# Performance work log

Hardware: AMD Instinct MI355X
Metric: run time of the kernel (lower is better)

Reference implementation:

```python
import jax, jax.numpy as jnp
import numpy as np

N_NODES = 50000   # batch_size * n_verts
N_EDGES = 800000
D_FEAT = 128
UNITS = 256


def setup_inputs() -> dict:
    key = jax.random.key(0)
    k1, k2, k3, k4, k5 = jax.random.split(key, 5)
    features = jax.random.normal(k1, (N_NODES, D_FEAT), dtype=jnp.float32)
    edge_row = jax.random.randint(k2, (N_EDGES,), 0, N_NODES, dtype=jnp.int32)
    edge_col = jax.random.randint(k3, (N_EDGES,), 0, N_NODES, dtype=jnp.int32)
    edge_val = jax.random.uniform(k4, (N_EDGES,), dtype=jnp.float32)
    W = jax.random.normal(k5, (D_FEAT, UNITS), dtype=jnp.float32) * (1.0 / np.sqrt(D_FEAT))
    return {"features": features, "edge_row": edge_row, "edge_col": edge_col,
            "edge_val": edge_val, "W": W}


def reference(features, edge_row, edge_col, edge_val, W):
    # features: [N, F] (already the (batch*n_verts, F) layout the layer reshapes to)
    # A in COO: A[edge_row[e], edge_col[e]] = edge_val[e]
    n = features.shape[0]
    # in_degree = row-sum of A values, +1 for self loop
    in_degree = jax.ops.segment_sum(edge_val, edge_row, num_segments=n) + 1.0
    invsqrt_deg = jax.lax.rsqrt(in_degree)                       # [N]
    normalized = invsqrt_deg[:, None] * features                 # [N, F]
    # pooled = A @ normalized  (gather source rows, scale, scatter-add to dest)
    msgs = edge_val[:, None] * normalized[edge_col]              # [E, F]
    pooled = jax.ops.segment_sum(msgs, edge_row, num_segments=n) # [N, F]
    # self-loop contribution (normalized case)
    pooled = pooled + invsqrt_deg[:, None] * normalized
    # dense projection + relu
    out = jax.nn.relu(pooled @ W)                                # [N, units]
    return out
```

## Files before the change

### kernel.cpp

```cpp
#include <hip/hip_runtime.h>

constexpr int N = 50000;
constexpr int E = 800000;
constexpr int F = 128;
constexpr int U = 256;

constexpr int R      = 8;
constexpr int CAP    = 16;
constexpr int ROWCAP = R * CAP;
constexpr int EBLK2  = (E + 511) / 512;

typedef __attribute__((ext_vector_type(8))) short short8;
typedef __attribute__((ext_vector_type(4))) float float4v;

__device__ inline unsigned short f32_to_bf16(float x) {
    unsigned int u = __float_as_uint(x);
    unsigned int r = (u + 0x7fffu + ((u >> 16) & 1u)) >> 16;
    return (unsigned short)r;
}
__device__ inline float bf_lo(unsigned int u) { return __uint_as_float(u << 16); }
__device__ inline float bf_hi(unsigned int u) { return __uint_as_float(u & 0xffff0000u); }

__global__ __launch_bounds__(256) void hist_kernel(const int* __restrict__ erow,
                                                   const int* __restrict__ ecol,
                                                   const float* __restrict__ eval,
                                                   int* __restrict__ cnt,
                                                   int2* __restrict__ csr,
                                                   const float* __restrict__ W,
                                                   unsigned short* __restrict__ Wt) {
    if (blockIdx.x >= EBLK2) {
        int idx = (blockIdx.x - EBLK2) * 256 + threadIdx.x;
        int k = idx >> 8;
        int n = idx & 255;
        Wt[n * F + k] = f32_to_bf16(W[idx]);
        return;
    }
    int e0  = blockIdx.x * 512 + threadIdx.x;
    int e1  = e0 + 256;
    int rep = blockIdx.x & (R - 1);
    bool h1 = (e1 < E);

    int   r0 = erow[e0];
    int   r1 = h1 ? erow[e1] : 0;
    int   c0 = ecol[e0];
    int   c1 = h1 ? ecol[e1] : 0;
    float v0 = eval[e0];
    float v1 = h1 ? eval[e1] : 0.f;

    int rk0 = atomicAdd(&cnt[r0 * R + rep], 1);
    int rk1 = h1 ? atomicAdd(&cnt[r1 * R + rep], 1) : CAP;

    if (rk0 < CAP)
        csr[(size_t)r0 * ROWCAP + rep * CAP + rk0] = make_int2(c0, __float_as_int(v0));
    if (rk1 < CAP)
        csr[(size_t)r1 * ROWCAP + rep * CAP + rk1] = make_int2(c1, __float_as_int(v1));
}

__global__ __launch_bounds__(256) void norm_kernel(const float* __restrict__ feat,
                                                   const int* __restrict__ cnt,
                                                   int2* __restrict__ csr,
                                                   int2* __restrict__ meta,
                                                   unsigned int* __restrict__ nrm) {
    int gtid = blockIdx.x * 256 + threadIdx.x;
    int n    = gtid >> 6;
    int lane = threadIdx.x & 63;
    if (n >= N) return;

    int s = lane >> 3;
    int j = lane & 7;

    int cval = min(cnt[n * R + (lane & 7)], CAP);
    int tot = 0, myoff = 0, cs = 0;
    #pragma unroll
    for (int t = 0; t < 8; ++t) {
        int ct = __shfl(cval, t, 64);
        tot += ct;
        if (t < s) myoff += ct;
        if (t == s) cs = ct;
    }

    int2* base = csr + (size_t)n * ROWCAP;
    bool h0 = j < cs;
    bool h1 = (j + 8) < cs;
    int2 v0 = h0 ? base[s * CAP + j] : make_int2(0, 0);
    int2 v1 = h1 ? base[s * CAP + 8 + j] : make_int2(0, 0);

    float sum = (h0 ? __int_as_float(v0.y) : 0.f) + (h1 ? __int_as_float(v1.y) : 0.f);
    #pragma unroll
    for (int off = 32; off > 0; off >>= 1) sum += __shfl_xor(sum, off, 64);
    float iv_ = rsqrtf(sum + 1.0f);

    if (h0) base[myoff + j] = v0;
    if (h1) base[myoff + 8 + j] = v1;

    if (lane == 0) meta[n] = make_int2(tot, __float_as_int(iv_));

    float2 f = ((const float2*)feat)[n * 64 + lane];
    nrm[n * 64 + lane] =
        (unsigned int)f32_to_bf16(iv_ * f.x) | ((unsigned int)f32_to_bf16(iv_ * f.y) << 16);
}

__global__ __launch_bounds__(256) void gather_kernel(const int2* __restrict__ meta,
                                                     const int2* __restrict__ csr,
                                                     const unsigned int* __restrict__ nrm,
                                                     unsigned int* __restrict__ pooledb) {
    int gtid = blockIdx.x * 256 + threadIdx.x;
    int n    = gtid >> 6;
    int lane = threadIdx.x & 63;
    if (n >= N) return;

    int2 m = meta[n];
    int tot = m.x;
    float iv_ = __int_as_float(m.y);

    unsigned int self = nrm[n * 64 + lane];
    float acc0 = iv_ * bf_lo(self);
    float acc1 = iv_ * bf_hi(self);

    const int2* base = csr + (size_t)n * ROWCAP;

    int e = 0;
    for (; e + 7 < tot; e += 8) {
        int2 p0 = base[e + 0], p1 = base[e + 1], p2 = base[e + 2], p3 = base[e + 3];
        int2 p4 = base[e + 4], p5 = base[e + 5], p6 = base[e + 6], p7 = base[e + 7];
        unsigned int u0 = nrm[(size_t)p0.x * 64 + lane];
        unsigned int u1 = nrm[(size_t)p1.x * 64 + lane];
        unsigned int u2 = nrm[(size_t)p2.x * 64 + lane];
        unsigned int u3 = nrm[(size_t)p3.x * 64 + lane];
        unsigned int u4 = nrm[(size_t)p4.x * 64 + lane];
        unsigned int u5 = nrm[(size_t)p5.x * 64 + lane];
        unsigned int u6 = nrm[(size_t)p6.x * 64 + lane];
        unsigned int u7 = nrm[(size_t)p7.x * 64 + lane];
        acc0 += __int_as_float(p0.y) * bf_lo(u0); acc1 += __int_as_float(p0.y) * bf_hi(u0);
        acc0 += __int_as_float(p1.y) * bf_lo(u1); acc1 += __int_as_float(p1.y) * bf_hi(u1);
        acc0 += __int_as_float(p2.y) * bf_lo(u2); acc1 += __int_as_float(p2.y) * bf_hi(u2);
        acc0 += __int_as_float(p3.y) * bf_lo(u3); acc1 += __int_as_float(p3.y) * bf_hi(u3);
        acc0 += __int_as_float(p4.y) * bf_lo(u4); acc1 += __int_as_float(p4.y) * bf_hi(u4);
        acc0 += __int_as_float(p5.y) * bf_lo(u5); acc1 += __int_as_float(p5.y) * bf_hi(u5);
        acc0 += __int_as_float(p6.y) * bf_lo(u6); acc1 += __int_as_float(p6.y) * bf_hi(u6);
        acc0 += __int_as_float(p7.y) * bf_lo(u7); acc1 += __int_as_float(p7.y) * bf_hi(u7);
    }
    for (; e + 3 < tot; e += 4) {
        int2 p0 = base[e + 0], p1 = base[e + 1], p2 = base[e + 2], p3 = base[e + 3];
        unsigned int u0 = nrm[(size_t)p0.x * 64 + lane];
        unsigned int u1 = nrm[(size_t)p1.x * 64 + lane];
        unsigned int u2 = nrm[(size_t)p2.x * 64 + lane];
        unsigned int u3 = nrm[(size_t)p3.x * 64 + lane];
        acc0 += __int_as_float(p0.y) * bf_lo(u0); acc1 += __int_as_float(p0.y) * bf_hi(u0);
        acc0 += __int_as_float(p1.y) * bf_lo(u1); acc1 += __int_as_float(p1.y) * bf_hi(u1);
        acc0 += __int_as_float(p2.y) * bf_lo(u2); acc1 += __int_as_float(p2.y) * bf_hi(u2);
        acc0 += __int_as_float(p3.y) * bf_lo(u3); acc1 += __int_as_float(p3.y) * bf_hi(u3);
    }
    for (; e < tot; ++e) {
        int2 p0 = base[e];
        unsigned int u0 = nrm[(size_t)p0.x * 64 + lane];
        acc0 += __int_as_float(p0.y) * bf_lo(u0);
        acc1 += __int_as_float(p0.y) * bf_hi(u0);
    }
    pooledb[n * 64 + lane] =
        (unsigned int)f32_to_bf16(acc0) | ((unsigned int)f32_to_bf16(acc1) << 16);
}

__global__ __launch_bounds__(256) void gemm_mfma_kernel(const unsigned short* __restrict__ Ab,
                                                        const unsigned short* __restrict__ Wt,
                                                        float* __restrict__ out) {
    __shared__ unsigned short As[16384];
    __shared__ unsigned short Bs[16384];
    const int tid = threadIdx.x;
    const int m0 = blockIdx.x * 128;
    const int n0 = blockIdx.y * 128;

    {
        const int r = tid >> 1;
        const int h = tid & 1;
        const int grow = m0 + r;
        const uint4* asrc = (grow < N) ? (const uint4*)(Ab + (size_t)grow * F) : nullptr;
        const uint4* bsrc = (const uint4*)(Wt + (size_t)(n0 + r) * F);
        #pragma unroll
        for (int j = 0; j < 8; ++j) {
            int o = h * 8 + j;
            int ks = o >> 2, quad = o & 3;
            int slot = ((ks * 8 + (r >> 4)) * 64) + (quad << 4) + (r & 15);
            uint4 av = asrc ? asrc[o] : make_uint4(0u, 0u, 0u, 0u);
            ((uint4*)As)[slot] = av;
            ((uint4*)Bs)[slot] = bsrc[o];
        }
    }
    __syncthreads();

    const int wave = tid >> 6;
    const int lane = tid & 63;
    float4v acc[8][2];
    #pragma unroll
    for (int i = 0; i < 8; ++i) {
        acc[i][0] = (float4v){0.f, 0.f, 0.f, 0.f};
        acc[i][1] = (float4v){0.f, 0.f, 0.f, 0.f};
    }

    #pragma unroll
    for (int ks = 0; ks < 4; ++ks) {
        short8 b0 = *(const short8*)&Bs[(((ks * 8 + wave * 2 + 0) * 64) + lane) * 8];
        short8 b1 = *(const short8*)&Bs[(((ks * 8 + wave * 2 + 1) * 64) + lane) * 8];
        #pragma unroll
        for (int mt = 0; mt < 8; ++mt) {
            short8 a = *(const short8*)&As[(((ks * 8 + mt) * 64) + lane) * 8];
            acc[mt][0] = __builtin_amdgcn_mfma_f32_16x16x32_bf16(a, b0, acc[mt][0], 0, 0, 0);
            acc[mt][1] = __builtin_amdgcn_mfma_f32_16x16x32_bf16(a, b1, acc[mt][1], 0, 0, 0);
        }
    }

    const int quad = lane >> 4;
    const int colt = lane & 15;
    #pragma unroll
    for (int mt = 0; mt < 8; ++mt) {
        #pragma unroll
        for (int nt = 0; nt < 2; ++nt) {
            int col = n0 + (wave * 2 + nt) * 16 + colt;
            #pragma unroll
            for (int i = 0; i < 4; ++i) {
                int row = m0 + mt * 16 + quad * 4 + i;
                if (row < N) out[(size_t)row * U + col] = fmaxf(acc[mt][nt][i], 0.f);
            }
        }
    }
}

extern "C" void kernel_launch(void* const* d_in, const int* in_sizes, int n_in,
                              void* d_out, int out_size, void* d_ws, size_t ws_size,
                              hipStream_t stream) {
    (void)in_sizes; (void)n_in; (void)out_size; (void)ws_size;

    const float* feat = (const float*)d_in[0];
    const int*   erow = (const int*)d_in[1];
    const int*   ecol = (const int*)d_in[2];
    const float* eval = (const float*)d_in[3];
    const float* W    = (const float*)d_in[4];
    float* out = (float*)d_out;

    char* ws = (char*)d_ws;
    int*            cnt     = (int*)  (ws + 0);
    int2*           meta    = (int2*) (ws + 1600000);
    unsigned short* Wt      = (unsigned short*)(ws + 2000000);
    unsigned int*   nrm     = (unsigned int*)  (ws + 2065536);
    unsigned int*   pooledb = (unsigned int*)  (ws + 14865536);
    int2*           csr     = (int2*) (ws + 27665536);

    (void)hipMemsetAsync(cnt, 0, (size_t)N * R * sizeof(int), stream);

    hist_kernel<<<EBLK2 + (F * U) / 256, 256, 0, stream>>>(erow, ecol, eval, cnt, csr, W, Wt);
    norm_kernel  <<<(N * 64) / 256, 256, 0, stream>>>(feat, cnt, csr, meta, nrm);
    gather_kernel<<<(N * 64) / 256, 256, 0, stream>>>(meta, csr, nrm, pooledb);

    dim3 ggrid((N + 127) / 128, U / 128);
    gemm_mfma_kernel<<<ggrid, 256, 0, stream>>>((const unsigned short*)pooledb, Wt, out);
}
```

Measured before the change: 211.9 us.

## Gather with 16-byte vector loads over four edge groups and wave shuffle reduction

The gather kernel now splits each 64-lane wavefront into four groups of 16 lanes. Each group handles a different edge and loads a full 256-byte feature row as uint4 per lane, then the partial sums are combined with xor shuffles. This cuts the number of memory instructions per edge and keeps more independent gathers in flight, at the cost of eight accumulators per lane and a shuffle reduction. The hist kernel also goes back to one edge per thread, which changes the replica assignment and launches twice as many blocks.

```diff
diff --git a/kernel.cpp b/kernel.cpp
--- a/kernel.cpp
+++ b/kernel.cpp
@@ -8,7 +8,7 @@
 constexpr int R      = 8;
 constexpr int CAP    = 16;
 constexpr int ROWCAP = R * CAP;
-constexpr int EBLK2  = (E + 511) / 512;
+constexpr int EBLK   = E / 256;
 
 typedef __attribute__((ext_vector_type(8))) short short8;
 typedef __attribute__((ext_vector_type(4))) float float4v;
@@ -28,32 +28,21 @@
                                                    int2* __restrict__ csr,
                                                    const float* __restrict__ W,
                                                    unsigned short* __restrict__ Wt) {
-    if (blockIdx.x >= EBLK2) {
-        int idx = (blockIdx.x - EBLK2) * 256 + threadIdx.x;
+    if (blockIdx.x >= EBLK) {
+        int idx = (blockIdx.x - EBLK) * 256 + threadIdx.x;
         int k = idx >> 8;
         int n = idx & 255;
         Wt[n * F + k] = f32_to_bf16(W[idx]);
         return;
     }
-    int e0  = blockIdx.x * 512 + threadIdx.x;
-    int e1  = e0 + 256;
+    int e   = blockIdx.x * 256 + threadIdx.x;
+    int row = erow[e];
+    int col = ecol[e];
+    float v = eval[e];
     int rep = blockIdx.x & (R - 1);
-    bool h1 = (e1 < E);
-
-    int   r0 = erow[e0];
-    int   r1 = h1 ? erow[e1] : 0;
-    int   c0 = ecol[e0];
-    int   c1 = h1 ? ecol[e1] : 0;
-    float v0 = eval[e0];
-    float v1 = h1 ? eval[e1] : 0.f;
-
-    int rk0 = atomicAdd(&cnt[r0 * R + rep], 1);
-    int rk1 = h1 ? atomicAdd(&cnt[r1 * R + rep], 1) : CAP;
-
-    if (rk0 < CAP)
-        csr[(size_t)r0 * ROWCAP + rep * CAP + rk0] = make_int2(c0, __float_as_int(v0));
-    if (rk1 < CAP)
-        csr[(size_t)r1 * ROWCAP + rep * CAP + rk1] = make_int2(c1, __float_as_int(v1));
+    int rk  = atomicAdd(&cnt[row * R + rep], 1);
+    if (rk < CAP)
+        csr[(size_t)row * ROWCAP + rep * CAP + rk] = make_int2(col, __float_as_int(v));
 }
 
 __global__ __launch_bounds__(256) void norm_kernel(const float* __restrict__ feat,
@@ -109,56 +98,68 @@
     int lane = threadIdx.x & 63;
     if (n >= N) return;
 
+    int q = lane >> 4;
+    int f = lane & 15;
+
     int2 m = meta[n];
     int tot = m.x;
     float iv_ = __int_as_float(m.y);
 
-    unsigned int self = nrm[n * 64 + lane];
-    float acc0 = iv_ * bf_lo(self);
-    float acc1 = iv_ * bf_hi(self);
-
-    const int2* base = csr + (size_t)n * ROWCAP;
+    const uint4* nrmv = (const uint4*)nrm;
+    const int2*  base = csr + (size_t)n * ROWCAP;
+
+    float acc[8] = {0.f, 0.f, 0.f, 0.f, 0.f, 0.f, 0.f, 0.f};
+
+    if (q == 0) {
+        uint4 u = nrmv[(size_t)n * 16 + f];
+        acc[0] = iv_ * bf_lo(u.x); acc[1] = iv_ * bf_hi(u.x);
+        acc[2] = iv_ * bf_lo(u.y); acc[3] = iv_ * bf_hi(u.y);
+        acc[4] = iv_ * bf_lo(u.z); acc[5] = iv_ * bf_hi(u.z);
+        acc[6] = iv_ * bf_lo(u.w); acc[7] = iv_ * bf_hi(u.w);
+    }
 
     int e = 0;
     for (; e + 7 < tot; e += 8) {
-        int2 p0 = base[e + 0], p1 = base[e + 1], p2 = base[e + 2], p3 = base[e + 3];
-        int2 p4 = base[e + 4], p5 = base[e + 5], p6 = base[e + 6], p7 = base[e + 7];
-        unsigned int u0 = nrm[(size_t)p0.x * 64 + lane];
-        unsigned int u1 = nrm[(size_t)p1.x * 64 + lane];
-        unsigned int u2 = nrm[(size_t)p2.x * 64 + lane];
-        unsigned int u3 = nrm[(size_t)p3.x * 64 + lane];
-        unsigned int u4 = nrm[(size_t)p4.x * 64 + lane];
-        unsigned int u5 = nrm[(size_t)p5.x * 64 + lane];
-        unsigned int u6 = nrm[(size_t)p6.x * 64 + lane];
-        unsigned int u7 = nrm[(size_t)p7.x * 64 + lane];
-        acc0 += __int_as_float(p0.y) * bf_lo(u0); acc1 += __int_as_float(p0.y) * bf_hi(u0);
-        acc0 += __int_as_float(p1.y) * bf_lo(u1); acc1 += __int_as_float(p1.y) * bf_hi(u1);
-        acc0 += __int_as_float(p2.y) * bf_lo(u2); acc1 += __int_as_float(p2.y) * bf_hi(u2);
-        acc0 += __int_as_float(p3.y) * bf_lo(u3); acc1 += __int_as_float(p3.y) * bf_hi(u3);
-        acc0 += __int_as_float(p4.y) * bf_lo(u4); acc1 += __int_as_float(p4.y) * bf_hi(u4);
-        acc0 += __int_as_float(p5.y) * bf_lo(u5); acc1 += __int_as_float(p5.y) * bf_hi(u5);
-        acc0 += __int_as_float(p6.y) * bf_lo(u6); acc1 += __int_as_float(p6.y) * bf_hi(u6);
-        acc0 += __int_as_float(p7.y) * bf_lo(u7); acc1 += __int_as_float(p7.y) * bf_hi(u7);
-    }
-    for (; e + 3 < tot; e += 4) {
-        int2 p0 = base[e + 0], p1 = base[e + 1], p2 = base[e + 2], p3 = base[e + 3];
-        unsigned int u0 = nrm[(size_t)p0.x * 64 + lane];
-        unsigned int u1 = nrm[(size_t)p1.x * 64 + lane];
-        unsigned int u2 = nrm[(size_t)p2.x * 64 + lane];
-        unsigned int u3 = nrm[(size_t)p3.x * 64 + lane];
-        acc0 += __int_as_float(p0.y) * bf_lo(u0); acc1 += __int_as_float(p0.y) * bf_hi(u0);
-        acc0 += __int_as_float(p1.y) * bf_lo(u1); acc1 += __int_as_float(p1.y) * bf_hi(u1);
-        acc0 += __int_as_float(p2.y) * bf_lo(u2); acc1 += __int_as_float(p2.y) * bf_hi(u2);
-        acc0 += __int_as_float(p3.y) * bf_lo(u3); acc1 += __int_as_float(p3.y) * bf_hi(u3);
-    }
-    for (; e < tot; ++e) {
-        int2 p0 = base[e];
-        unsigned int u0 = nrm[(size_t)p0.x * 64 + lane];
-        acc0 += __int_as_float(p0.y) * bf_lo(u0);
-        acc1 += __int_as_float(p0.y) * bf_hi(u0);
-    }
-    pooledb[n * 64 + lane] =
-        (unsigned int)f32_to_bf16(acc0) | ((unsigned int)f32_to_bf16(acc1) << 16);
+        int2 pa = base[e + q];
+        int2 pb = base[e + 4 + q];
+        float va = __int_as_float(pa.y);
+        float vb = __int_as_float(pb.y);
+        uint4 ua = nrmv[(size_t)pa.x * 16 + f];
+        uint4 ub = nrmv[(size_t)pb.x * 16 + f];
+        acc[0] += va * bf_lo(ua.x); acc[1] += va * bf_hi(ua.x);
+        acc[2] += va * bf_lo(ua.y); acc[3] += va * bf_hi(ua.y);
+        acc[4] += va * bf_lo(ua.z); acc[5] += va * bf_hi(ua.z);
+        acc[6] += va * bf_lo(ua.w); acc[7] += va * bf_hi(ua.w);
+        acc[0] += vb * bf_lo(ub.x); acc[1] += vb * bf_hi(ub.x);
+        acc[2] += vb * bf_lo(ub.y); acc[3] += vb * bf_hi(ub.y);
+        acc[4] += vb * bf_lo(ub.z); acc[5] += vb * bf_hi(ub.z);
+        acc[6] += vb * bf_lo(ub.w); acc[7] += vb * bf_hi(ub.w);
+    }
+    for (; e < tot; e += 4) {
+        bool ok = (e + q) < tot;
+        int2 p = ok ? base[e + q] : make_int2(0, 0);
+        float v = __int_as_float(p.y);
+        uint4 u = nrmv[(size_t)p.x * 16 + f];
+        acc[0] += v * bf_lo(u.x); acc[1] += v * bf_hi(u.x);
+        acc[2] += v * bf_lo(u.y); acc[3] += v * bf_hi(u.y);
+        acc[4] += v * bf_lo(u.z); acc[5] += v * bf_hi(u.z);
+        acc[6] += v * bf_lo(u.w); acc[7] += v * bf_hi(u.w);
+    }
+
+    #pragma unroll
+    for (int i = 0; i < 8; ++i) {
+        acc[i] += __shfl_xor(acc[i], 16, 64);
+        acc[i] += __shfl_xor(acc[i], 32, 64);
+    }
+
+    if (q == 0) {
+        uint4 o;
+        o.x = (unsigned int)f32_to_bf16(acc[0]) | ((unsigned int)f32_to_bf16(acc[1]) << 16);
+        o.y = (unsigned int)f32_to_bf16(acc[2]) | ((unsigned int)f32_to_bf16(acc[3]) << 16);
+        o.z = (unsigned int)f32_to_bf16(acc[4]) | ((unsigned int)f32_to_bf16(acc[5]) << 16);
+        o.w = (unsigned int)f32_to_bf16(acc[6]) | ((unsigned int)f32_to_bf16(acc[7]) << 16);
+        ((uint4*)pooledb)[(size_t)n * 16 + f] = o;
+    }
 }
 
 __global__ __launch_bounds__(256) void gemm_mfma_kernel(const unsigned short* __restrict__ Ab,
@@ -247,7 +248,7 @@
 
     (void)hipMemsetAsync(cnt, 0, (size_t)N * R * sizeof(int), stream);
 
-    hist_kernel<<<EBLK2 + (F * U) / 256, 256, 0, stream>>>(erow, ecol, eval, cnt, csr, W, Wt);
+    hist_kernel<<<EBLK + (F * U) / 256, 256, 0, stream>>>(erow, ecol, eval, cnt, csr, W, Wt);
     norm_kernel  <<<(N * 64) / 256, 256, 0, stream>>>(feat, cnt, csr, meta, nrm);
     gather_kernel<<<(N * 64) / 256, 256, 0, stream>>>(meta, csr, nrm, pooledb);
 
```

Result: faster. 205.3 us (median of 2 runs) (-3.1%).
